# Performance work log

Measured on AMD Instinct MI355X. Metric: run time of the kernel, lower is better.

The kernel has to match this reference:

```python
import jax, jax.numpy as jnp
import numpy as np

BITS = 4
MAXQ = (1 << BITS) - 1          # 15
PACK = 32 // BITS               # 8 values per int32
IN_F = 4096
OUT_F = 11008


def setup_inputs() -> dict:
    key = jax.random.key(0)
    k1, k2, k3, k4, k5 = jax.random.split(key, 5)
    x = jax.random.normal(k1, (8, IN_F), dtype=jnp.float32)
    qweight = jax.random.randint(k2, (IN_F // 32 * BITS, OUT_F), 0, 2147483647, dtype=jnp.int32)
    qzeros = jax.random.randint(k3, (1, OUT_F // 32 * BITS), 0, 2147483647, dtype=jnp.int32)
    scales = jax.random.uniform(k4, (1, OUT_F), dtype=jnp.float32, minval=1e-3, maxval=2e-2)
    bias = jax.random.normal(k5, (OUT_F,), dtype=jnp.float32)
    return {"x": x, "qweight": qweight, "qzeros": qzeros, "scales": scales, "bias": bias}


def reference(x, qweight, qzeros, scales, bias):
    # GPTQ-style unpack: each int32 packs PACK values of BITS bits, LSB first.
    shifts = jnp.arange(0, 32, BITS, dtype=jnp.int32)  # wf
    # unpack weights: (IN_F//PACK, OUT_F) -> (IN_F//PACK, PACK, OUT_F) -> (IN_F, OUT_F)
    w = (qweight[:, None, :] >> shifts[None, :, None]) & MAXQ
    w = w.reshape(IN_F, OUT_F).astype(scales.dtype)
    # unpack zeros: (1, OUT_F//PACK) -> (1, OUT_F//PACK, PACK) -> (1, OUT_F), +1 per GPTQ convention
    z = ((qzeros[:, :, None] >> shifts[None, None, :]) & MAXQ) + 1
    z = z.reshape(1, OUT_F).astype(scales.dtype)
    # single quantization group (group_size == infeatures, g_idx all zeros)
    W = scales * (w - z)                      # (IN_F, OUT_F)
    return x @ W + bias
```

## Files before the change

### kernel.cpp

```cpp
#include <hip/hip_runtime.h>

#define IN_F 4096
#define OUT_F 11008
#define M 8
#define NWAVE 4
#define KPW (IN_F / NWAVE)
#define STEPS (KPW / 32)

typedef __bf16 bf16x8 __attribute__((ext_vector_type(8)));
typedef float  f32x4  __attribute__((ext_vector_type(4)));

__global__ __launch_bounds__(256, 4) void gptq_fused_kernel(
    const int*   __restrict__ qw,
    const float* __restrict__ x,
    const int*   __restrict__ qz,
    const float* __restrict__ sc,
    const float* __restrict__ bias,
    float*       __restrict__ out)
{
    __shared__ float red[NWAVE][M][16];

    const int bid  = (int)blockIdx.x;
    const int cpx  = (int)gridDim.x >> 3;
    const int tile = (bid & 7) * cpx + (bid >> 3);

    const int lane = (int)threadIdx.x & 63;
    const int w    = (int)threadIdx.x >> 6;
    const int t    = lane & 15;
    const int quad = lane >> 4;
    const int col  = tile * 16 + t;
    const int k0   = w * KPW;

    const float zf = (float)(((qz[col >> 3] >> ((col & 7) * 4)) & 15) + 1);

    int qv[STEPS];
    const int* qp = qw + (size_t)(k0 / 8 + quad) * OUT_F + col;
#pragma unroll
    for (int s = 0; s < STEPS; ++s)
        qv[s] = qp[(size_t)s * 4 * OUT_F];

    const float* xp = x + (size_t)(t & 7) * IN_F + k0 + quad * 8;

    f32x4 acc = {0.f, 0.f, 0.f, 0.f};

#pragma unroll
    for (int s = 0; s < STEPS; ++s) {
        union { unsigned int u[4]; bf16x8 v; } a;
        const float4 v0 = *(const float4*)(xp + s * 32);
        const float4 v1 = *(const float4*)(xp + s * 32 + 4);
        a.u[0] = (__float_as_uint(v0.x) >> 16) | (__float_as_uint(v0.y) & 0xffff0000u);
        a.u[1] = (__float_as_uint(v0.z) >> 16) | (__float_as_uint(v0.w) & 0xffff0000u);
        a.u[2] = (__float_as_uint(v1.x) >> 16) | (__float_as_uint(v1.y) & 0xffff0000u);
        a.u[3] = (__float_as_uint(v1.z) >> 16) | (__float_as_uint(v1.w) & 0xffff0000u);

        const unsigned q  = (unsigned)qv[s];
        const unsigned lo = q & 0x0f0f0f0fu;
        const unsigned hi = (q >> 4) & 0x0f0f0f0fu;
        union { unsigned int u[4]; bf16x8 v; } b;
#pragma unroll
        for (int p = 0; p < 4; ++p) {
            const float f0 = (float)((lo >> (8 * p)) & 0xffu) - zf;
            const float f1 = (float)((hi >> (8 * p)) & 0xffu) - zf;
            b.u[p] = (__float_as_uint(f0) >> 16) | (__float_as_uint(f1) & 0xffff0000u);
        }

        acc = __builtin_amdgcn_mfma_f32_16x16x32_bf16(a.v, b.v, acc, 0, 0, 0);
    }

    if (quad < 2) {
#pragma unroll
        for (int r = 0; r < 4; ++r)
            red[w][quad * 4 + r][t] = acc[r];
    }
    __syncthreads();

    if (threadIdx.x < M * 16) {
        const int r = (int)threadIdx.x >> 4;
        const int c = (int)threadIdx.x & 15;
        float sacc = 0.f;
#pragma unroll
        for (int i = 0; i < NWAVE; ++i) sacc += red[i][r][c];
        const int j = tile * 16 + c;
        out[(size_t)r * OUT_F + j] = fmaf(sc[j], sacc, bias[j]);
    }
}

extern "C" void kernel_launch(void* const* d_in, const int* in_sizes, int n_in,
                              void* d_out, int out_size, void* d_ws, size_t ws_size,
                              hipStream_t stream) {
    const float* x    = (const float*)d_in[0];
    const int*   qw   = (const int*)d_in[1];
    const int*   qz   = (const int*)d_in[2];
    const float* sc   = (const float*)d_in[3];
    const float* bias = (const float*)d_in[4];

    hipLaunchKernelGGL(gptq_fused_kernel, dim3(OUT_F / 16), dim3(256), 0, stream,
                       qw, x, qz, sc, bias, (float*)d_out);
}
```

Measured before the change: 95.77 us.

## Split-K across blocks with workspace partials and separate reduce kernel

Replaces the per-block four-wave in-block K split with a 2D grid of 16 K-slices. Each wave now owns its own 16 columns, and partial sums go to a global workspace. A second kernel sums the 16 partials and applies scale and bias. Byte packing to bf16 now uses v_perm instead of shift/or. This raises parallelism and coalesces each wave's qweight reads over 64 columns per block, at the cost of an extra launch and partial-sum traffic through global memory.

```diff
diff --git a/kernel.cpp b/kernel.cpp
--- a/kernel.cpp
+++ b/kernel.cpp
@@ -3,86 +3,91 @@
 #define IN_F 4096
 #define OUT_F 11008
 #define M 8
-#define NWAVE 4
-#define KPW (IN_F / NWAVE)
-#define STEPS (KPW / 32)
+#define S_SLICES 16
+#define KPS (IN_F / S_SLICES)
+#define RPSL (KPS / 8)
+#define STEPS (KPS / 32)
 
 typedef __bf16 bf16x8 __attribute__((ext_vector_type(8)));
 typedef float  f32x4  __attribute__((ext_vector_type(4)));
 
-__global__ __launch_bounds__(256, 4) void gptq_fused_kernel(
+__device__ __forceinline__ unsigned pack_bf_trunc(float lo, float hi) {
+    return __builtin_amdgcn_perm(__float_as_uint(hi), __float_as_uint(lo),
+                                 0x07060302u);
+}
+
+__global__ __launch_bounds__(256, 4) void gptq_mfma_fused(
     const int*   __restrict__ qw,
     const float* __restrict__ x,
     const int*   __restrict__ qz,
-    const float* __restrict__ sc,
-    const float* __restrict__ bias,
-    float*       __restrict__ out)
+    float*       __restrict__ P)
 {
-    __shared__ float red[NWAVE][M][16];
-
-    const int bid  = (int)blockIdx.x;
-    const int cpx  = (int)gridDim.x >> 3;
-    const int tile = (bid & 7) * cpx + (bid >> 3);
-
     const int lane = (int)threadIdx.x & 63;
-    const int w    = (int)threadIdx.x >> 6;
+    const int wv   = (int)threadIdx.x >> 6;
     const int t    = lane & 15;
     const int quad = lane >> 4;
-    const int col  = tile * 16 + t;
-    const int k0   = w * KPW;
+    const int col  = ((int)blockIdx.x * 4 + wv) * 16 + t;
+    const int i0   = (int)blockIdx.y * RPSL;
+    const int kb   = (int)blockIdx.y * KPS;
 
     const float zf = (float)(((qz[col >> 3] >> ((col & 7) * 4)) & 15) + 1);
 
     int qv[STEPS];
-    const int* qp = qw + (size_t)(k0 / 8 + quad) * OUT_F + col;
+    const int* qp = qw + (size_t)(i0 + quad) * OUT_F + col;
 #pragma unroll
     for (int s = 0; s < STEPS; ++s)
         qv[s] = qp[(size_t)s * 4 * OUT_F];
 
-    const float* xp = x + (size_t)(t & 7) * IN_F + k0 + quad * 8;
+    const float* xp = x + (size_t)(t & 7) * IN_F + kb + quad * 8;
 
     f32x4 acc = {0.f, 0.f, 0.f, 0.f};
 
 #pragma unroll
     for (int s = 0; s < STEPS; ++s) {
-        union { unsigned int u[4]; bf16x8 v; } a;
+        union { unsigned u[4]; bf16x8 v; } a;
         const float4 v0 = *(const float4*)(xp + s * 32);
         const float4 v1 = *(const float4*)(xp + s * 32 + 4);
-        a.u[0] = (__float_as_uint(v0.x) >> 16) | (__float_as_uint(v0.y) & 0xffff0000u);
-        a.u[1] = (__float_as_uint(v0.z) >> 16) | (__float_as_uint(v0.w) & 0xffff0000u);
-        a.u[2] = (__float_as_uint(v1.x) >> 16) | (__float_as_uint(v1.y) & 0xffff0000u);
-        a.u[3] = (__float_as_uint(v1.z) >> 16) | (__float_as_uint(v1.w) & 0xffff0000u);
+        a.u[0] = pack_bf_trunc(v0.x, v0.y);
+        a.u[1] = pack_bf_trunc(v0.z, v0.w);
+        a.u[2] = pack_bf_trunc(v1.x, v1.y);
+        a.u[3] = pack_bf_trunc(v1.z, v1.w);
 
         const unsigned q  = (unsigned)qv[s];
         const unsigned lo = q & 0x0f0f0f0fu;
         const unsigned hi = (q >> 4) & 0x0f0f0f0fu;
-        union { unsigned int u[4]; bf16x8 v; } b;
+        union { unsigned u[4]; bf16x8 v; } b;
 #pragma unroll
         for (int p = 0; p < 4; ++p) {
             const float f0 = (float)((lo >> (8 * p)) & 0xffu) - zf;
             const float f1 = (float)((hi >> (8 * p)) & 0xffu) - zf;
-            b.u[p] = (__float_as_uint(f0) >> 16) | (__float_as_uint(f1) & 0xffff0000u);
+            b.u[p] = pack_bf_trunc(f0, f1);
         }
 
         acc = __builtin_amdgcn_mfma_f32_16x16x32_bf16(a.v, b.v, acc, 0, 0, 0);
     }
 
     if (quad < 2) {
+        float* Pp = P + (size_t)blockIdx.y * (M * OUT_F);
+        const int r0 = quad * 4;
 #pragma unroll
         for (int r = 0; r < 4; ++r)
-            red[w][quad * 4 + r][t] = acc[r];
+            Pp[(size_t)(r0 + r) * OUT_F + col] = acc[r];
     }
-    __syncthreads();
+}
 
-    if (threadIdx.x < M * 16) {
-        const int r = (int)threadIdx.x >> 4;
-        const int c = (int)threadIdx.x & 15;
-        float sacc = 0.f;
+__global__ __launch_bounds__(64) void gptq_reduce(
+    const float* __restrict__ P, const float* __restrict__ sc,
+    const float* __restrict__ bias, float* __restrict__ out)
+{
+    const int r = (int)blockIdx.y;
+    const int j = (int)blockIdx.x * 64 + (int)threadIdx.x;
+
+    float acc = 0.0f;
 #pragma unroll
-        for (int i = 0; i < NWAVE; ++i) sacc += red[i][r][c];
-        const int j = tile * 16 + c;
-        out[(size_t)r * OUT_F + j] = fmaf(sc[j], sacc, bias[j]);
-    }
+    for (int s = 0; s < S_SLICES; ++s)
+        acc += P[(size_t)s * (M * OUT_F) + (size_t)r * OUT_F + j];
+
+    out[(size_t)r * OUT_F + j] = fmaf(sc[j], acc, bias[j]);
 }
 
 extern "C" void kernel_launch(void* const* d_in, const int* in_sizes, int n_in,
@@ -93,7 +98,12 @@
     const int*   qz   = (const int*)d_in[2];
     const float* sc   = (const float*)d_in[3];
     const float* bias = (const float*)d_in[4];
+    float* out = (float*)d_out;
 
-    hipLaunchKernelGGL(gptq_fused_kernel, dim3(OUT_F / 16), dim3(256), 0, stream,
-                       qw, x, qz, sc, bias, (float*)d_out);
+    float* P = (float*)d_ws;
+
+    hipLaunchKernelGGL(gptq_mfma_fused, dim3(OUT_F / 64, S_SLICES), dim3(256), 0,
+                       stream, qw, x, qz, P);
+    hipLaunchKernelGGL(gptq_reduce, dim3(OUT_F / 64, M), dim3(64), 0, stream,
+                       P, sc, bias, out);
 }
```

After: 95.83 us. About the same (+0.1%).
